# Optimization experiments

Measured on AMD Instinct MI355X. Metric: run time of the kernel, lower is better.

## Reference

```python
import jax, jax.numpy as jnp
import numpy as np

H = W = 256
WS = 8          # window size
SHIFT = 4       # shift size
HEADS = 8
DIM = 128
HD = DIM // HEADS
EPS = 1e-5


def _rel_index():
    # Swin-style relative position index, static constant (N=WS*WS)
    coords = np.stack(np.meshgrid(np.arange(WS), np.arange(WS), indexing='ij')).reshape(2, -1)
    rel = coords[:, :, None] - coords[:, None, :]        # (2, N, N)
    rel = rel + (WS - 1)
    return rel[0] * (2 * WS - 1) + rel[1]                # (N, N) in [0, (2WS-1)^2)

_REL_IDX = _rel_index()


def _ln(x, w, b):
    m = jnp.mean(x, axis=-1, keepdims=True)
    v = jnp.var(x, axis=-1, keepdims=True)
    return (x - m) * jax.lax.rsqrt(v + EPS) * w + b


def setup_inputs() -> dict:
    key = jax.random.key(0)
    ks = jax.random.split(key, 8)
    s = 0.02
    return {
        'x': jax.random.normal(ks[0], (2, H * W, DIM), jnp.float32),
        'norm1_w': jnp.ones((DIM,), jnp.float32),
        'norm1_b': jnp.zeros((DIM,), jnp.float32),
        'qkv_w': jax.random.normal(ks[1], (3 * DIM, DIM), jnp.float32) * s,
        'qkv_b': jnp.zeros((3 * DIM,), jnp.float32),
        'rel_bias_table': jax.random.normal(ks[2], ((2 * WS - 1) ** 2, HEADS), jnp.float32) * s,
        'proj_w': jax.random.normal(ks[3], (DIM, DIM), jnp.float32) * s,
        'proj_b': jnp.zeros((DIM,), jnp.float32),
        'norm2_w': jnp.ones((DIM,), jnp.float32),
        'norm2_b': jnp.zeros((DIM,), jnp.float32),
        'fc1_w': jax.random.normal(ks[4], (4 * DIM, DIM), jnp.float32) * s,
        'fc1_b': jnp.zeros((4 * DIM,), jnp.float32),
        'fc2_w': jax.random.normal(ks[5], (DIM, 4 * DIM), jnp.float32) * s,
        'fc2_b': jnp.zeros((DIM,), jnp.float32),
    }


def reference(x, norm1_w, norm1_b, qkv_w, qkv_b, rel_bias_table, proj_w, proj_b,
              norm2_w, norm2_b, fc1_w, fc1_b, fc2_w, fc2_b):
    B, L, C = x.shape
    N = WS * WS
    shortcut = x

    # norm1 -> spatial -> shift (roll only; original applies no attention mask)
    xs = _ln(x, norm1_w, norm1_b).reshape(B, H, W, C)
    xs = jnp.roll(xs, shift=(-SHIFT, -SHIFT), axis=(1, 2))

    # window partition: (B*nH*nW, N, C)
    win = xs.reshape(B, H // WS, WS, W // WS, WS, C)
    win = win.transpose(0, 1, 3, 2, 4, 5).reshape(-1, N, C)

    # window attention
    qkv = (win @ qkv_w.T + qkv_b).reshape(-1, N, 3, HEADS, HD)
    qkv = qkv.transpose(2, 0, 3, 1, 4)                   # (3, nWin, heads, N, hd)
    q, k, v = qkv[0], qkv[1], qkv[2]
    scale = HD ** -0.5
    attn = jnp.einsum('whnd,whmd->whnm', q * scale, k)   # (nWin, heads, N, N)
    bias = rel_bias_table[_REL_IDX]                      # (N, N, heads)
    attn = attn + bias.transpose(2, 0, 1)[None]
    attn = jax.nn.softmax(attn, axis=-1)
    out = jnp.einsum('whnm,whmd->whnd', attn, v)         # (nWin, heads, N, hd)
    out = out.transpose(0, 2, 1, 3).reshape(-1, N, C)
    out = out @ proj_w.T + proj_b

    # window reverse + un-shift
    out = out.reshape(B, H // WS, W // WS, WS, WS, C)
    out = out.transpose(0, 1, 3, 2, 4, 5).reshape(B, H, W, C)
    out = jnp.roll(out, shift=(SHIFT, SHIFT), axis=(1, 2)).reshape(B, L, C)

    x = shortcut + out

    # MLP (fc1 -> exact GELU -> fc2) with residual
    h = _ln(x, norm2_w, norm2_b)
    h = jax.nn.gelu(h @ fc1_w.T + fc1_b, approximate=False)
    h = h @ fc2_w.T + fc2_b
    return x + h
```

## Files before the change

### kernel.cpp

```cpp
#include <hip/hip_runtime.h>
#include <hip/hip_bf16.h>
#include <cmath>

#define LNEPS 1e-5f

typedef __attribute__((ext_vector_type(8))) short short8v;
typedef __attribute__((ext_vector_type(4))) float f32x4;

__device__ __forceinline__ unsigned short f2bf(float f){
  unsigned u = __float_as_uint(f);
  u += 0x7fffu + ((u >> 16) & 1u);
  return (unsigned short)(u >> 16);
}
__device__ __forceinline__ float gelu_f(float x){
  return 0.5f * x * (1.f + erff(x * 0.70710678118654752f));
}

__device__ __forceinline__ f32x4 mfma32(short8v a, short8v b, f32x4 c){
#ifdef __HIP_DEVICE_COMPILE__
  return __builtin_amdgcn_mfma_f32_16x16x32_bf16(a, b, c, 0, 0, 0);
#else
  return c;
#endif
}

__device__ __forceinline__ void stage128(const unsigned short* g, int ldg, short* lds){
#ifdef __HIP_DEVICE_COMPILE__
  const int t = threadIdx.x;
  const int wv = t >> 6;
  #pragma unroll
  for (int it = 0; it < 8; ++it) {
    const int flat = it * 256 + t;
    const int r = flat >> 4, c = flat & 15;
    const unsigned short* src = g + (size_t)r * ldg + ((c ^ (r & 7)) << 3);
    short* dst = lds + (size_t)(it * 256 + wv * 64) * 8;
    __builtin_amdgcn_global_load_lds(
        (const __attribute__((address_space(1))) void*)src,
        (__attribute__((address_space(3))) void*)dst, 16, 0, 0);
  }
#else
  (void)g; (void)ldg; (void)lds;
#endif
}
__device__ __forceinline__ void stage64(const unsigned short* g, short* lds){
#ifdef __HIP_DEVICE_COMPILE__
  const int t = threadIdx.x;
  const int wv = t >> 6;
  #pragma unroll
  for (int it = 0; it < 4; ++it) {
    const int flat = it * 256 + t;
    const int r = flat >> 4, c = flat & 15;
    const unsigned short* src = g + (size_t)r * 128 + ((c ^ (r & 7)) << 3);
    short* dst = lds + (size_t)(it * 256 + wv * 64) * 8;
    __builtin_amdgcn_global_load_lds(
        (const __attribute__((address_space(1))) void*)src,
        (__attribute__((address_space(3))) void*)dst, 16, 0, 0);
  }
#else
  (void)g; (void)lds;
#endif
}
__device__ __forceinline__ short8v frag_ld(const short* lds, int row, int chunk){
  return *(const short8v*)((const char*)lds + row * 256 + ((chunk ^ (row & 7)) << 4));
}

__global__ __launch_bounds__(256) void k0_cvt(
    const float* __restrict__ qkvw, const float* __restrict__ pw,
    const float* __restrict__ w1, const float* __restrict__ w2,
    unsigned short* __restrict__ dst)
{
  const int i = (blockIdx.x * 256 + threadIdx.x) * 4;
  const float* src; int off;
  if (i < 49152)       { src = qkvw; off = i; }
  else if (i < 65536)  { src = pw;   off = i - 49152; }
  else if (i < 131072) { src = w1;   off = i - 65536; }
  else                 { src = w2;   off = i - 131072; }
  const float4 v = *(const float4*)(src + off);
  ushort4 o = { f2bf(v.x), f2bf(v.y), f2bf(v.z), f2bf(v.w) };
  *(ushort4*)(dst + i) = o;
}

__global__ __launch_bounds__(256, 2) void k2_qkv(
    const float* __restrict__ x,
    const float* __restrict__ gw, const float* __restrict__ gb,
    const unsigned short* __restrict__ Wb,
    const float* __restrict__ bias,
    unsigned short* __restrict__ qk,
    unsigned short* __restrict__ vt)
{
  __shared__ __align__(16) short At[128 * 128];
  __shared__ __align__(16) short Bt[128 * 128];
  const int t = threadIdx.x;
  const int row0 = blockIdx.x * 128;
  stage128(Wb, 128, At);
  #pragma unroll
  for (int it = 0; it < 8; ++it) {
    const int flat = it * 256 + t;
    const int r = flat >> 4, c = flat & 15;
    const int row = row0 + r;
    const int wid = row >> 6, n = row & 63;
    const int b = wid >> 10, rem = wid & 1023;
    const int wh = rem >> 5, wwi = rem & 31;
    const int i = n >> 3, j = n & 7;
    const int sh = (wh * 8 + i + 4) & 255;
    const int sw = (wwi * 8 + j + 4) & 255;
    const float* src = x + (((size_t)b << 16) + sh * 256 + sw) * 128 + c * 8;
    const float4 a0 = *(const float4*)src;
    const float4 a1 = *(const float4*)(src + 4);
    float s  = a0.x + a0.y + a0.z + a0.w + a1.x + a1.y + a1.z + a1.w;
    float ss = a0.x*a0.x + a0.y*a0.y + a0.z*a0.z + a0.w*a0.w
             + a1.x*a1.x + a1.y*a1.y + a1.z*a1.z + a1.w*a1.w;
    s += __shfl_xor(s, 1); ss += __shfl_xor(ss, 1);
    s += __shfl_xor(s, 2); ss += __shfl_xor(ss, 2);
    s += __shfl_xor(s, 4); ss += __shfl_xor(ss, 4);
    s += __shfl_xor(s, 8); ss += __shfl_xor(ss, 8);
    const float mean = s * 0.0078125f;
    const float rstd = rsqrtf(ss * 0.0078125f - mean * mean + LNEPS);
    const float4 g0 = *(const float4*)(gw + c * 8), g1 = *(const float4*)(gw + c * 8 + 4);
    const float4 c0 = *(const float4*)(gb + c * 8), c1 = *(const float4*)(gb + c * 8 + 4);
    uint4 pk;
    pk.x = (unsigned)f2bf((a0.x - mean) * rstd * g0.x + c0.x)
         | ((unsigned)f2bf((a0.y - mean) * rstd * g0.y + c0.y) << 16);
    pk.y = (unsigned)f2bf((a0.z - mean) * rstd * g0.z + c0.z)
         | ((unsigned)f2bf((a0.w - mean) * rstd * g0.w + c0.w) << 16);
    pk.z = (unsigned)f2bf((a1.x - mean) * rstd * g1.x + c1.x)
         | ((unsigned)f2bf((a1.y - mean) * rstd * g1.y + c1.y) << 16);
    pk.w = (unsigned)f2bf((a1.z - mean) * rstd * g1.z + c1.z)
         | ((unsigned)f2bf((a1.w - mean) * rstd * g1.w + c1.w) << 16);
    *(uint4*)((char*)Bt + r * 256 + ((c ^ (r & 7)) << 4)) = pk;
  }
  __syncthreads();

  const int l = t & 63, w = t >> 6, w0 = w & 1, w1 = w >> 1;
  const int g = l >> 4, rl = l & 15;
  const f32x4 z = {0.f, 0.f, 0.f, 0.f};

  for (int nt = 0; nt < 3; ++nt) {
    f32x4 acc[4][4];
    #pragma unroll
    for (int i = 0; i < 4; ++i)
      #pragma unroll
      for (int j = 0; j < 4; ++j) acc[i][j] = z;
    #pragma unroll
    for (int kk = 0; kk < 4; ++kk) {
      short8v a[4], b[4];
      #pragma unroll
      for (int i = 0; i < 4; ++i) a[i] = frag_ld(At, w0 * 64 + i * 16 + rl, kk * 4 + g);
      #pragma unroll
      for (int j = 0; j < 4; ++j) b[j] = frag_ld(Bt, w1 * 64 + j * 16 + rl, kk * 4 + g);
      #pragma unroll
      for (int i = 0; i < 4; ++i)
        #pragma unroll
        for (int j = 0; j < 4; ++j)
          acc[i][j] = mfma32(a[i], b[j], acc[i][j]);
    }
    if (nt < 2) {
      const int n0 = nt * 128;
      #pragma unroll
      for (int i = 0; i < 4; ++i) {
        const int np = w0 * 64 + i * 16 + 4 * g;
        const float4 bv = *(const float4*)(bias + n0 + np);
        #pragma unroll
        for (int j = 0; j < 4; ++j) {
          const int r = row0 + w1 * 64 + j * 16 + rl;
          ushort4 o = { f2bf(acc[i][j][0] + bv.x), f2bf(acc[i][j][1] + bv.y),
                        f2bf(acc[i][j][2] + bv.z), f2bf(acc[i][j][3] + bv.w) };
          *(ushort4*)(qk + (size_t)r * 256 + n0 + np) = o;
        }
      }
    } else {
      #pragma unroll
      for (int i = 0; i < 4; ++i) {
        const int np = w0 * 64 + i * 16 + 4 * g;
        const int h = np >> 4, db = np & 15;
        const float4 bv = *(const float4*)(bias + 256 + np);
        const float ba[4] = {bv.x, bv.y, bv.z, bv.w};
        #pragma unroll
        for (int j = 0; j < 4; ++j) {
          const int r = row0 + w1 * 64 + j * 16 + rl;
          const int wn = r >> 6, m = r & 63;
          unsigned short* dst = vt + (((size_t)wn * 8 + h) << 10) + m;
          #pragma unroll
          for (int e = 0; e < 4; ++e)
            dst[(db + e) * 64] = f2bf(acc[i][j][e] + ba[e]);
        }
      }
    }
    if (nt < 2) {
      __syncthreads();
      stage128(Wb + (size_t)(nt + 1) * 16384, 128, At);
      __syncthreads();
    }
  }
}

__global__ __launch_bounds__(256, 2) void k3_attn(
    const unsigned short* __restrict__ qk,
    const unsigned short* __restrict__ vt,
    const float* __restrict__ table,
    unsigned short* __restrict__ attn)
{
  __shared__ float Tb[1800];
  __shared__ __align__(16) unsigned short Pl[4][4096];
  const int t = threadIdx.x;
  for (int i = t; i < 1800; i += 256) Tb[i] = table[i];
  __syncthreads();
  const int l = t & 63, w = t >> 6;
  const int id = blockIdx.x * 4 + w;
  const int win = id >> 3, h = id & 7;
  const int g = l >> 4, rl = l & 15;
  const unsigned short* qbase = qk + (size_t)win * 64 * 256 + h * 16;
  const short8v zz = {0,0,0,0,0,0,0,0};
  short8v qf[4], kf[4];
  if (g < 2) {
    #pragma unroll
    for (int rf = 0; rf < 4; ++rf)
      qf[rf] = *(const short8v*)(qbase + (size_t)(rf * 16 + rl) * 256 + g * 8);
    #pragma unroll
    for (int mf = 0; mf < 4; ++mf)
      kf[mf] = *(const short8v*)(qbase + 128 + (size_t)(mf * 16 + rl) * 256 + g * 8);
  } else {
    #pragma unroll
    for (int i = 0; i < 4; ++i) { qf[i] = zz; kf[i] = zz; }
  }
  const f32x4 z = {0.f, 0.f, 0.f, 0.f};
  f32x4 s[4][4];
  #pragma unroll
  for (int mf = 0; mf < 4; ++mf)
    #pragma unroll
    for (int rf = 0; rf < 4; ++rf)
      s[mf][rf] = mfma32(kf[mf], qf[rf], z);
  float sum[4];
  #pragma unroll
  for (int rf = 0; rf < 4; ++rf) {
    const int r = rf * 16 + rl, i1 = r >> 3, j1 = r & 7;
    float mx = -1e30f;
    #pragma unroll
    for (int mf = 0; mf < 4; ++mf)
      #pragma unroll
      for (int e = 0; e < 4; ++e) {
        const int m = mf * 16 + g * 4 + e;
        const int i2 = m >> 3, j2 = m & 7;
        const float v = s[mf][rf][e] * 0.25f + Tb[((i1 - i2 + 7) * 15 + (j1 - j2 + 7)) * 8 + h];
        s[mf][rf][e] = v;
        mx = fmaxf(mx, v);
      }
    mx = fmaxf(mx, __shfl_xor(mx, 16));
    mx = fmaxf(mx, __shfl_xor(mx, 32));
    float sm = 0.f;
    #pragma unroll
    for (int mf = 0; mf < 4; ++mf)
      #pragma unroll
      for (int e = 0; e < 4; ++e) {
        const float ev = __expf(s[mf][rf][e] - mx);
        s[mf][rf][e] = ev;
        sm += ev;
      }
    sm += __shfl_xor(sm, 16);
    sm += __shfl_xor(sm, 32);
    sum[rf] = sm;
  }
  char* Pw = (char*)&Pl[w][0];
  #pragma unroll
  for (int rf = 0; rf < 4; ++rf) {
    const int r = rf * 16 + rl;
    const int swz = (r & 7) << 4;
    #pragma unroll
    for (int mf = 0; mf < 4; ++mf) {
      uint2 u;
      u.x = (unsigned)f2bf(s[mf][rf][0]) | ((unsigned)f2bf(s[mf][rf][1]) << 16);
      u.y = (unsigned)f2bf(s[mf][rf][2]) | ((unsigned)f2bf(s[mf][rf][3]) << 16);
      *(uint2*)(Pw + ((r * 128 + mf * 32 + g * 8) ^ swz)) = u;
    }
  }
  const unsigned short* vb = vt + (((size_t)win * 8 + h) << 10) + rl * 64 + g * 8;
  f32x4 o[4];
  #pragma unroll
  for (int rf = 0; rf < 4; ++rf) o[rf] = z;
  #pragma unroll
  for (int c = 0; c < 2; ++c) {
    const short8v va = *(const short8v*)(vb + c * 32);
    #pragma unroll
    for (int rf = 0; rf < 4; ++rf) {
      const int r = rf * 16 + rl;
      const short8v pb = *(const short8v*)(Pw + ((r * 128 + c * 64 + g * 16) ^ ((r & 7) << 4)));
      o[rf] = mfma32(va, pb, o[rf]);
    }
  }
  #pragma unroll
  for (int rf = 0; rf < 4; ++rf) {
    const float inv = 1.f / sum[rf];
    const int r = rf * 16 + rl;
    ushort4 ov = { f2bf(o[rf][0] * inv), f2bf(o[rf][1] * inv),
                   f2bf(o[rf][2] * inv), f2bf(o[rf][3] * inv) };
    *(ushort4*)(attn + ((size_t)win * 64 + r) * 128 + h * 16 + g * 4) = ov;
  }
}

__global__ __launch_bounds__(256, 2) void k45_proj_mlp(
    const unsigned short* __restrict__ A,
    const unsigned short* __restrict__ pwb,
    const float* __restrict__ pb,
    const float* __restrict__ xin,
    const float* __restrict__ gw, const float* __restrict__ gb,
    const unsigned short* __restrict__ w1b, const float* __restrict__ b1,
    const unsigned short* __restrict__ w2b, const float* __restrict__ b2,
    float* __restrict__ out)
{
  __shared__ __align__(16) short Xt[64 * 128];
  __shared__ __align__(16) short Ht[64 * 128];
  __shared__ __align__(16) short Wt[128 * 128];
  __shared__ float2 Gt[1024];
  __shared__ float2 Red[64 * 8];
  const int t = threadIdx.x;
  const int row0 = blockIdx.x * 64;
  stage128(pwb, 128, Wt);
  stage64(A + (size_t)row0 * 128, Ht);
  #pragma unroll
  for (int i = t; i < 1024; i += 256) {
    const float x0 = (float)i * 0.0078125f - 4.f;
    const float g0 = gelu_f(x0);
    Gt[i] = make_float2(g0, gelu_f(x0 + 0.0078125f) - g0);
  }
  const int l = t & 63, w = t >> 6, w0 = w & 1, w1 = w >> 1;
  const int g = l >> 4, rl = l & 15;
  size_t obase[2];
  float4 xv[4][2];
  #pragma unroll
  for (int j = 0; j < 2; ++j) {
    const int r = row0 + w1 * 32 + j * 16 + rl;
    const int wn = r >> 6, n = r & 63;
    const int b_ = wn >> 10, rem = wn & 1023;
    const int wh = rem >> 5, ww = rem & 31;
    const int si = n >> 3, sj = n & 7;
    const int hd = (wh * 8 + si + 4) & 255;
    const int wd = (ww * 8 + sj + 4) & 255;
    obase[j] = (((size_t)b_ << 16) + hd * 256 + wd) * 128;
    #pragma unroll
    for (int i = 0; i < 4; ++i)
      xv[i][j] = *(const float4*)(xin + obase[j] + w0 * 64 + i * 16 + 4 * g);
  }
  __syncthreads();
  const f32x4 z = {0.f, 0.f, 0.f, 0.f};
  f32x4 x2r[4][2];
  #pragma unroll
  for (int i = 0; i < 4; ++i) { x2r[i][0] = z; x2r[i][1] = z; }
  #pragma unroll
  for (int kk = 0; kk < 4; ++kk) {
    short8v a[4], b[2];
    #pragma unroll
    for (int i = 0; i < 4; ++i) a[i] = frag_ld(Wt, w0 * 64 + i * 16 + rl, kk * 4 + g);
    #pragma unroll
    for (int j = 0; j < 2; ++j) b[j] = frag_ld(Ht, w1 * 32 + j * 16 + rl, kk * 4 + g);
    #pragma unroll
    for (int i = 0; i < 4; ++i)
      #pragma unroll
      for (int j = 0; j < 2; ++j)
        x2r[i][j] = mfma32(a[i], b[j], x2r[i][j]);
  }
  #pragma unroll
  for (int i = 0; i < 4; ++i) {
    const float4 bv = *(const float4*)(pb + w0 * 64 + i * 16 + 4 * g);
    #pragma unroll
    for (int j = 0; j < 2; ++j) {
      x2r[i][j][0] += xv[i][j].x + bv.x;
      x2r[i][j][1] += xv[i][j].y + bv.y;
      x2r[i][j][2] += xv[i][j].z + bv.z;
      x2r[i][j][3] += xv[i][j].w + bv.w;
    }
  }
  #pragma unroll
  for (int j = 0; j < 2; ++j) {
    float s = 0.f, ss = 0.f;
    #pragma unroll
    for (int i = 0; i < 4; ++i)
      #pragma unroll
      for (int e = 0; e < 4; ++e) { const float v = x2r[i][j][e]; s += v; ss += v * v; }
    Red[(w1 * 32 + j * 16 + rl) * 8 + (w0 * 4 + g)] = make_float2(s, ss);
  }
  __syncthreads();
  float mean[2], rstd[2];
  #pragma unroll
  for (int j = 0; j < 2; ++j) {
    const float2* rp = &Red[(w1 * 32 + j * 16 + rl) * 8];
    float s = 0.f, ss = 0.f;
    #pragma unroll
    for (int k = 0; k < 8; ++k) { s += rp[k].x; ss += rp[k].y; }
    mean[j] = s * 0.0078125f;
    rstd[j] = rsqrtf(ss * 0.0078125f - mean[j] * mean[j] + LNEPS);
  }
  #pragma unroll
  for (int i = 0; i < 4; ++i) {
    const int c = w0 * 64 + i * 16 + 4 * g;
    const float4 g4 = *(const float4*)(gw + c);
    const float4 c4 = *(const float4*)(gb + c);
    #pragma unroll
    for (int j = 0; j < 2; ++j) {
      const int r = w1 * 32 + j * 16 + rl;
      ushort4 p;
      p.x = f2bf((x2r[i][j][0] - mean[j]) * rstd[j] * g4.x + c4.x);
      p.y = f2bf((x2r[i][j][1] - mean[j]) * rstd[j] * g4.y + c4.y);
      p.z = f2bf((x2r[i][j][2] - mean[j]) * rstd[j] * g4.z + c4.z);
      p.w = f2bf((x2r[i][j][3] - mean[j]) * rstd[j] * g4.w + c4.w);
      const int chunk = c >> 3, inner = (c & 7) * 2;
      *(ushort4*)((char*)Xt + r * 256 + ((chunk ^ (r & 7)) << 4) + inner) = p;
    }
  }
  f32x4 oacc[4][2];
  #pragma unroll
  for (int i = 0; i < 4; ++i) { oacc[i][0] = z; oacc[i][1] = z; }
  for (int sb = 0; sb < 4; ++sb) {
    __syncthreads();
    stage128(w1b + (size_t)sb * 128 * 128, 128, Wt);
    __syncthreads();
    f32x4 hacc[4][2];
    #pragma unroll
    for (int i = 0; i < 4; ++i) { hacc[i][0] = z; hacc[i][1] = z; }
    #pragma unroll
    for (int kk = 0; kk < 4; ++kk) {
      short8v a[4], b[2];
      #pragma unroll
      for (int i = 0; i < 4; ++i) a[i] = frag_ld(Wt, w0 * 64 + i * 16 + rl, kk * 4 + g);
      #pragma unroll
      for (int j = 0; j < 2; ++j) b[j] = frag_ld(Xt, w1 * 32 + j * 16 + rl, kk * 4 + g);
      #pragma unroll
      for (int i = 0; i < 4; ++i)
        #pragma unroll
        for (int j = 0; j < 2; ++j)
          hacc[i][j] = mfma32(a[i], b[j], hacc[i][j]);
    }
    __syncthreads();
    #pragma unroll
    for (int i = 0; i < 4; ++i) {
      const int cl = w0 * 64 + i * 16 + 4 * g;
      const float4 b1v = *(const float4*)(b1 + sb * 128 + cl);
      const float ba[4] = {b1v.x, b1v.y, b1v.z, b1v.w};
      #pragma unroll
      for (int j = 0; j < 2; ++j) {
        const int r = w1 * 32 + j * 16 + rl;
        unsigned short pe[4];
        #pragma unroll
        for (int e = 0; e < 4; ++e) {
          const float xh = hacc[i][j][e] + ba[e];
          float tq = fmaf(xh, 128.f, 512.f);
          tq = fminf(fmaxf(tq, 0.f), 1023.99f);
          const float fi = floorf(tq);
          const float2 ent = Gt[(int)fi];
          float gv = fmaf(tq - fi, ent.y, ent.x);
          gv = xh > 3.98f ? xh : gv;
          pe[e] = f2bf(gv);
        }
        ushort4 p = { pe[0], pe[1], pe[2], pe[3] };
        const int chunk = cl >> 3, inner = (cl & 7) * 2;
        *(ushort4*)((char*)Ht + r * 256 + ((chunk ^ (r & 7)) << 4) + inner) = p;
      }
    }
    stage128(w2b + (size_t)sb * 128, 512, Wt);
    __syncthreads();
    #pragma unroll
    for (int kk = 0; kk < 4; ++kk) {
      short8v a[4], b[2];
      #pragma unroll
      for (int i = 0; i < 4; ++i) a[i] = frag_ld(Wt, w0 * 64 + i * 16 + rl, kk * 4 + g);
      #pragma unroll
      for (int j = 0; j < 2; ++j) b[j] = frag_ld(Ht, w1 * 32 + j * 16 + rl, kk * 4 + g);
      #pragma unroll
      for (int i = 0; i < 4; ++i)
        #pragma unroll
        for (int j = 0; j < 2; ++j)
          oacc[i][j] = mfma32(a[i], b[j], oacc[i][j]);
    }
  }
  #pragma unroll
  for (int i = 0; i < 4; ++i) {
    const int c = w0 * 64 + i * 16 + 4 * g;
    const float4 bv = *(const float4*)(b2 + c);
    #pragma unroll
    for (int j = 0; j < 2; ++j) {
      float4 o = { x2r[i][j][0] + oacc[i][j][0] + bv.x,
                   x2r[i][j][1] + oacc[i][j][1] + bv.y,
                   x2r[i][j][2] + oacc[i][j][2] + bv.z,
                   x2r[i][j][3] + oacc[i][j][3] + bv.w };
      *(float4*)(out + obase[j] + c) = o;
    }
  }
}

extern "C" void kernel_launch(void* const* d_in, const int* in_sizes, int n_in,
                              void* d_out, int out_size, void* d_ws, size_t ws_size,
                              hipStream_t stream)
{
  const float* x    = (const float*)d_in[0];
  const float* n1w  = (const float*)d_in[1];
  const float* n1b  = (const float*)d_in[2];
  const float* qkvw = (const float*)d_in[3];
  const float* qkvB = (const float*)d_in[4];
  const float* relb = (const float*)d_in[5];
  const float* pw   = (const float*)d_in[6];
  const float* pb   = (const float*)d_in[7];
  const float* n2w  = (const float*)d_in[8];
  const float* n2b  = (const float*)d_in[9];
  const float* w1   = (const float*)d_in[10];
  const float* b1   = (const float*)d_in[11];
  const float* w2   = (const float*)d_in[12];
  const float* b2   = (const float*)d_in[13];
  float* out = (float*)d_out;

  unsigned short* winb = (unsigned short*)d_ws;
  unsigned short* qkb  = winb + 16777216;
  unsigned short* vtb  = qkb + 33554432;
  unsigned short* wb   = vtb + 16777216;
  unsigned short* qkvw_b = wb;
  unsigned short* pw_b   = wb + 49152;
  unsigned short* w1_b   = wb + 65536;
  unsigned short* w2_b   = wb + 131072;

  k0_cvt<<<192, 256, 0, stream>>>(qkvw, pw, w1, w2, wb);
  k2_qkv<<<1024, 256, 0, stream>>>(x, n1w, n1b, qkvw_b, qkvB, qkb, vtb);
  k3_attn<<<4096, 256, 0, stream>>>(qkb, vtb, relb, winb);
  k45_proj_mlp<<<2048, 256, 0, stream>>>(winb, pw_b, pb, x, n2w, n2b,
                                         w1_b, b1, w2_b, b2, out);
}
```

Measured before the change: 182.3 us.

## Fuse QKV projection and window attention into one kernel via LDS

Merges the QKV GEMM kernel and the attention kernel so that Q/K and transposed V stay in shared memory instead of round-tripping through global memory. Blocks grow to 512 threads covering two windows, with 8 waves each handling one head after the GEMM. Attention reuses the At and Bt buffers for P and V. This removes large intermediate global writes and reads plus one launch. In exchange, LDS use per block rises to about 135KB, which limits occupancy to one block per CU.

```diff
diff --git a/kernel.cpp b/kernel.cpp
--- a/kernel.cpp
+++ b/kernel.cpp
@@ -34,6 +34,24 @@
     const int r = flat >> 4, c = flat & 15;
     const unsigned short* src = g + (size_t)r * ldg + ((c ^ (r & 7)) << 3);
     short* dst = lds + (size_t)(it * 256 + wv * 64) * 8;
+    __builtin_amdgcn_global_load_lds(
+        (const __attribute__((address_space(1))) void*)src,
+        (__attribute__((address_space(3))) void*)dst, 16, 0, 0);
+  }
+#else
+  (void)g; (void)ldg; (void)lds;
+#endif
+}
+__device__ __forceinline__ void stage128_512(const unsigned short* g, int ldg, short* lds){
+#ifdef __HIP_DEVICE_COMPILE__
+  const int t = threadIdx.x;
+  const int wv = t >> 6;
+  #pragma unroll
+  for (int it = 0; it < 4; ++it) {
+    const int flat = it * 512 + t;
+    const int r = flat >> 4, c = flat & 15;
+    const unsigned short* src = g + (size_t)r * ldg + ((c ^ (r & 7)) << 3);
+    short* dst = lds + (size_t)(it * 512 + wv * 64) * 8;
     __builtin_amdgcn_global_load_lds(
         (const __attribute__((address_space(1))) void*)src,
         (__attribute__((address_space(3))) void*)dst, 16, 0, 0);
@@ -80,30 +98,33 @@
   *(ushort4*)(dst + i) = o;
 }
 
-__global__ __launch_bounds__(256, 2) void k2_qkv(
+__global__ __launch_bounds__(512, 2) void k23_qkv_attn(
     const float* __restrict__ x,
     const float* __restrict__ gw, const float* __restrict__ gb,
     const unsigned short* __restrict__ Wb,
     const float* __restrict__ bias,
-    unsigned short* __restrict__ qk,
-    unsigned short* __restrict__ vt)
+    const float* __restrict__ table,
+    unsigned short* __restrict__ attn)
 {
   __shared__ __align__(16) short At[128 * 128];
   __shared__ __align__(16) short Bt[128 * 128];
+  __shared__ __align__(16) short QKl[128 * 256];
+  __shared__ float Tb[1800];
   const int t = threadIdx.x;
   const int row0 = blockIdx.x * 128;
-  stage128(Wb, 128, At);
-  #pragma unroll
-  for (int it = 0; it < 8; ++it) {
-    const int flat = it * 256 + t;
+  stage128_512(Wb, 128, At);
+  for (int i = t; i < 1800; i += 512) Tb[i] = table[i];
+  #pragma unroll
+  for (int it = 0; it < 4; ++it) {
+    const int flat = it * 512 + t;
     const int r = flat >> 4, c = flat & 15;
     const int row = row0 + r;
     const int wid = row >> 6, n = row & 63;
     const int b = wid >> 10, rem = wid & 1023;
     const int wh = rem >> 5, wwi = rem & 31;
-    const int i = n >> 3, j = n & 7;
-    const int sh = (wh * 8 + i + 4) & 255;
-    const int sw = (wwi * 8 + j + 4) & 255;
+    const int i2 = n >> 3, j2 = n & 7;
+    const int sh = (wh * 8 + i2 + 4) & 255;
+    const int sw = (wwi * 8 + j2 + 4) & 255;
     const float* src = x + (((size_t)b << 16) + sh * 256 + sw) * 128 + c * 8;
     const float4 a0 = *(const float4*)src;
     const float4 a1 = *(const float4*)(src + 4);
@@ -136,164 +157,155 @@
   const f32x4 z = {0.f, 0.f, 0.f, 0.f};
 
   for (int nt = 0; nt < 3; ++nt) {
-    f32x4 acc[4][4];
-    #pragma unroll
-    for (int i = 0; i < 4; ++i)
-      #pragma unroll
-      for (int j = 0; j < 4; ++j) acc[i][j] = z;
+    f32x4 acc[4][2];
+    #pragma unroll
+    for (int i = 0; i < 4; ++i) { acc[i][0] = z; acc[i][1] = z; }
     #pragma unroll
     for (int kk = 0; kk < 4; ++kk) {
-      short8v a[4], b[4];
+      short8v a[4], b[2];
       #pragma unroll
       for (int i = 0; i < 4; ++i) a[i] = frag_ld(At, w0 * 64 + i * 16 + rl, kk * 4 + g);
       #pragma unroll
-      for (int j = 0; j < 4; ++j) b[j] = frag_ld(Bt, w1 * 64 + j * 16 + rl, kk * 4 + g);
+      for (int j = 0; j < 2; ++j) b[j] = frag_ld(Bt, w1 * 32 + j * 16 + rl, kk * 4 + g);
       #pragma unroll
       for (int i = 0; i < 4; ++i)
         #pragma unroll
-        for (int j = 0; j < 4; ++j)
+        for (int j = 0; j < 2; ++j)
           acc[i][j] = mfma32(a[i], b[j], acc[i][j]);
     }
     if (nt < 2) {
-      const int n0 = nt * 128;
       #pragma unroll
       for (int i = 0; i < 4; ++i) {
-        const int np = w0 * 64 + i * 16 + 4 * g;
-        const float4 bv = *(const float4*)(bias + n0 + np);
-        #pragma unroll
-        for (int j = 0; j < 4; ++j) {
-          const int r = row0 + w1 * 64 + j * 16 + rl;
+        const int c = w0 * 64 + i * 16 + 4 * g;
+        const float4 bv = *(const float4*)(bias + nt * 128 + c);
+        const int chunk = nt * 16 + (c >> 3), inner = (c & 7) * 2;
+        #pragma unroll
+        for (int j = 0; j < 2; ++j) {
+          const int r = w1 * 32 + j * 16 + rl;
           ushort4 o = { f2bf(acc[i][j][0] + bv.x), f2bf(acc[i][j][1] + bv.y),
                         f2bf(acc[i][j][2] + bv.z), f2bf(acc[i][j][3] + bv.w) };
-          *(ushort4*)(qk + (size_t)r * 256 + n0 + np) = o;
+          *(ushort4*)((char*)QKl + r * 512 + ((chunk ^ (r & 7)) << 4) + inner) = o;
         }
       }
+      __syncthreads();
+      stage128_512(Wb + (size_t)(nt + 1) * 16384, 128, At);
+      __syncthreads();
     } else {
+      __syncthreads();
       #pragma unroll
       for (int i = 0; i < 4; ++i) {
-        const int np = w0 * 64 + i * 16 + 4 * g;
-        const int h = np >> 4, db = np & 15;
-        const float4 bv = *(const float4*)(bias + 256 + np);
+        const int c = w0 * 64 + i * 16 + 4 * g;
+        const int h2 = c >> 4, db = c & 15;
+        const float4 bv = *(const float4*)(bias + 256 + c);
         const float ba[4] = {bv.x, bv.y, bv.z, bv.w};
         #pragma unroll
-        for (int j = 0; j < 4; ++j) {
-          const int r = row0 + w1 * 64 + j * 16 + rl;
-          const int wn = r >> 6, m = r & 63;
-          unsigned short* dst = vt + (((size_t)wn * 8 + h) << 10) + m;
+        for (int j = 0; j < 2; ++j) {
+          const int r = w1 * 32 + j * 16 + rl;
+          const int wl = r >> 6, m = r & 63;
+          char* vb = (char*)Bt + (wl * 8 + h2) * 2048;
           #pragma unroll
-          for (int e = 0; e < 4; ++e)
-            dst[(db + e) * 64] = f2bf(acc[i][j][e] + ba[e]);
+          for (int e = 0; e < 4; ++e) {
+            const int d = db + e;
+            *(unsigned short*)(vb + d * 128 + (((m >> 3) ^ (d & 7)) << 4) + (m & 7) * 2)
+                = f2bf(acc[i][j][e] + ba[e]);
+          }
         }
       }
-    }
-    if (nt < 2) {
       __syncthreads();
-      stage128(Wb + (size_t)(nt + 1) * 16384, 128, At);
-      __syncthreads();
-    }
-  }
-}
-
-__global__ __launch_bounds__(256, 2) void k3_attn(
-    const unsigned short* __restrict__ qk,
-    const unsigned short* __restrict__ vt,
-    const float* __restrict__ table,
-    unsigned short* __restrict__ attn)
-{
-  __shared__ float Tb[1800];
-  __shared__ __align__(16) unsigned short Pl[4][4096];
-  const int t = threadIdx.x;
-  for (int i = t; i < 1800; i += 256) Tb[i] = table[i];
-  __syncthreads();
-  const int l = t & 63, w = t >> 6;
-  const int id = blockIdx.x * 4 + w;
-  const int win = id >> 3, h = id & 7;
-  const int g = l >> 4, rl = l & 15;
-  const unsigned short* qbase = qk + (size_t)win * 64 * 256 + h * 16;
+    }
+  }
+
+  const int h = w;
+  char* Pw = (char*)At + w * 4096;
   const short8v zz = {0,0,0,0,0,0,0,0};
-  short8v qf[4], kf[4];
-  if (g < 2) {
-    #pragma unroll
-    for (int rf = 0; rf < 4; ++rf)
-      qf[rf] = *(const short8v*)(qbase + (size_t)(rf * 16 + rl) * 256 + g * 8);
+  for (int wl = 0; wl < 2; ++wl) {
+    const int win = blockIdx.x * 2 + wl;
+    short8v qf[4], kf[4];
+    if (g < 2) {
+      #pragma unroll
+      for (int rf = 0; rf < 4; ++rf) {
+        const int r = wl * 64 + rf * 16 + rl;
+        qf[rf] = *(const short8v*)((char*)QKl + r * 512 + (((2 * h + g) ^ (r & 7)) << 4));
+      }
+      #pragma unroll
+      for (int mf = 0; mf < 4; ++mf) {
+        const int r = wl * 64 + mf * 16 + rl;
+        kf[mf] = *(const short8v*)((char*)QKl + r * 512 + (((16 + 2 * h + g) ^ (r & 7)) << 4));
+      }
+    } else {
+      #pragma unroll
+      for (int i = 0; i < 4; ++i) { qf[i] = zz; kf[i] = zz; }
+    }
+    f32x4 s[4][4];
     #pragma unroll
     for (int mf = 0; mf < 4; ++mf)
-      kf[mf] = *(const short8v*)(qbase + 128 + (size_t)(mf * 16 + rl) * 256 + g * 8);
-  } else {
-    #pragma unroll
-    for (int i = 0; i < 4; ++i) { qf[i] = zz; kf[i] = zz; }
-  }
-  const f32x4 z = {0.f, 0.f, 0.f, 0.f};
-  f32x4 s[4][4];
-  #pragma unroll
-  for (int mf = 0; mf < 4; ++mf)
-    #pragma unroll
-    for (int rf = 0; rf < 4; ++rf)
-      s[mf][rf] = mfma32(kf[mf], qf[rf], z);
-  float sum[4];
-  #pragma unroll
-  for (int rf = 0; rf < 4; ++rf) {
-    const int r = rf * 16 + rl, i1 = r >> 3, j1 = r & 7;
-    float mx = -1e30f;
-    #pragma unroll
-    for (int mf = 0; mf < 4; ++mf)
-      #pragma unroll
-      for (int e = 0; e < 4; ++e) {
-        const int m = mf * 16 + g * 4 + e;
-        const int i2 = m >> 3, j2 = m & 7;
-        const float v = s[mf][rf][e] * 0.25f + Tb[((i1 - i2 + 7) * 15 + (j1 - j2 + 7)) * 8 + h];
-        s[mf][rf][e] = v;
-        mx = fmaxf(mx, v);
-      }
-    mx = fmaxf(mx, __shfl_xor(mx, 16));
-    mx = fmaxf(mx, __shfl_xor(mx, 32));
-    float sm = 0.f;
-    #pragma unroll
-    for (int mf = 0; mf < 4; ++mf)
-      #pragma unroll
-      for (int e = 0; e < 4; ++e) {
-        const float ev = __expf(s[mf][rf][e] - mx);
-        s[mf][rf][e] = ev;
-        sm += ev;
-      }
-    sm += __shfl_xor(sm, 16);
-    sm += __shfl_xor(sm, 32);
-    sum[rf] = sm;
-  }
-  char* Pw = (char*)&Pl[w][0];
-  #pragma unroll
-  for (int rf = 0; rf < 4; ++rf) {
-    const int r = rf * 16 + rl;
-    const int swz = (r & 7) << 4;
-    #pragma unroll
-    for (int mf = 0; mf < 4; ++mf) {
-      uint2 u;
-      u.x = (unsigned)f2bf(s[mf][rf][0]) | ((unsigned)f2bf(s[mf][rf][1]) << 16);
-      u.y = (unsigned)f2bf(s[mf][rf][2]) | ((unsigned)f2bf(s[mf][rf][3]) << 16);
-      *(uint2*)(Pw + ((r * 128 + mf * 32 + g * 8) ^ swz)) = u;
-    }
-  }
-  const unsigned short* vb = vt + (((size_t)win * 8 + h) << 10) + rl * 64 + g * 8;
-  f32x4 o[4];
-  #pragma unroll
-  for (int rf = 0; rf < 4; ++rf) o[rf] = z;
-  #pragma unroll
-  for (int c = 0; c < 2; ++c) {
-    const short8v va = *(const short8v*)(vb + c * 32);
+      #pragma unroll
+      for (int rf = 0; rf < 4; ++rf)
+        s[mf][rf] = mfma32(kf[mf], qf[rf], z);
+    float sum[4];
     #pragma unroll
     for (int rf = 0; rf < 4; ++rf) {
+      const int r = rf * 16 + rl, i1 = r >> 3, j1 = r & 7;
+      float mx = -1e30f;
+      #pragma unroll
+      for (int mf = 0; mf < 4; ++mf)
+        #pragma unroll
+        for (int e = 0; e < 4; ++e) {
+          const int m = mf * 16 + g * 4 + e;
+          const int i2 = m >> 3, j2 = m & 7;
+          const float v = s[mf][rf][e] * 0.25f + Tb[((i1 - i2 + 7) * 15 + (j1 - j2 + 7)) * 8 + h];
+          s[mf][rf][e] = v;
+          mx = fmaxf(mx, v);
+        }
+      mx = fmaxf(mx, __shfl_xor(mx, 16));
+      mx = fmaxf(mx, __shfl_xor(mx, 32));
+      float sm = 0.f;
+      #pragma unroll
+      for (int mf = 0; mf < 4; ++mf)
+        #pragma unroll
+        for (int e = 0; e < 4; ++e) {
+          const float ev = __expf(s[mf][rf][e] - mx);
+          s[mf][rf][e] = ev;
+          sm += ev;
+        }
+      sm += __shfl_xor(sm, 16);
+      sm += __shfl_xor(sm, 32);
+      sum[rf] = sm;
+    }
+    const char* vbase = (char*)Bt + (wl * 8 + h) * 2048;
+    f32x4 o[4];
+    #pragma unroll
+    for (int rf = 0; rf < 4; ++rf) o[rf] = z;
+    #pragma unroll
+    for (int hm = 0; hm < 2; ++hm) {
+      #pragma unroll
+      for (int rf = 0; rf < 4; ++rf) {
+        const int r = rf * 16 + rl;
+        #pragma unroll
+        for (int mfl = 0; mfl < 2; ++mfl) {
+          const int mf = hm * 2 + mfl;
+          uint2 u;
+          u.x = (unsigned)f2bf(s[mf][rf][0]) | ((unsigned)f2bf(s[mf][rf][1]) << 16);
+          u.y = (unsigned)f2bf(s[mf][rf][2]) | ((unsigned)f2bf(s[mf][rf][3]) << 16);
+          *(uint2*)(Pw + r * 64 + (((mfl * 2 + (g >> 1)) ^ ((r >> 1) & 3)) << 4) + (g & 1) * 8) = u;
+        }
+      }
+      const short8v va = *(const short8v*)(vbase + rl * 128 + (((hm * 4 + g) ^ (rl & 7)) << 4));
+      #pragma unroll
+      for (int rf = 0; rf < 4; ++rf) {
+        const int r = rf * 16 + rl;
+        const short8v pb = *(const short8v*)(Pw + r * 64 + ((g ^ ((r >> 1) & 3)) << 4));
+        o[rf] = mfma32(va, pb, o[rf]);
+      }
+    }
+    #pragma unroll
+    for (int rf = 0; rf < 4; ++rf) {
+      const float inv = 1.f / sum[rf];
       const int r = rf * 16 + rl;
-      const short8v pb = *(const short8v*)(Pw + ((r * 128 + c * 64 + g * 16) ^ ((r & 7) << 4)));
-      o[rf] = mfma32(va, pb, o[rf]);
-    }
-  }
-  #pragma unroll
-  for (int rf = 0; rf < 4; ++rf) {
-    const float inv = 1.f / sum[rf];
-    const int r = rf * 16 + rl;
-    ushort4 ov = { f2bf(o[rf][0] * inv), f2bf(o[rf][1] * inv),
-                   f2bf(o[rf][2] * inv), f2bf(o[rf][3] * inv) };
-    *(ushort4*)(attn + ((size_t)win * 64 + r) * 128 + h * 16 + g * 4) = ov;
+      ushort4 ov = { f2bf(o[rf][0] * inv), f2bf(o[rf][1] * inv),
+                     f2bf(o[rf][2] * inv), f2bf(o[rf][3] * inv) };
+      *(ushort4*)(attn + ((size_t)win * 64 + r) * 128 + h * 16 + g * 4) = ov;
+    }
   }
 }
 
@@ -507,17 +519,14 @@
   float* out = (float*)d_out;
 
   unsigned short* winb = (unsigned short*)d_ws;
-  unsigned short* qkb  = winb + 16777216;
-  unsigned short* vtb  = qkb + 33554432;
-  unsigned short* wb   = vtb + 16777216;
+  unsigned short* wb   = winb + 16777216;
   unsigned short* qkvw_b = wb;
   unsigned short* pw_b   = wb + 49152;
   unsigned short* w1_b   = wb + 65536;
   unsigned short* w2_b   = wb + 131072;
 
   k0_cvt<<<192, 256, 0, stream>>>(qkvw, pw, w1, w2, wb);
-  k2_qkv<<<1024, 256, 0, stream>>>(x, n1w, n1b, qkvw_b, qkvB, qkb, vtb);
-  k3_attn<<<4096, 256, 0, stream>>>(qkb, vtb, relb, winb);
+  k23_qkv_attn<<<1024, 512, 0, stream>>>(x, n1w, n1b, qkvw_b, qkvB, relb, winb);
   k45_proj_mlp<<<2048, 256, 0, stream>>>(winb, pw_b, pb, x, n2w, n2b,
                                          w1_b, b1, w2_b, b2, out);
 }
```

After: 177.2 us. 1.03x faster.
